# Optimization experiments

Hardware: AMD Instinct MI355X
Metric: run time of the kernel (lower is better)

The kernel has to match this reference:

```python
import jax, jax.numpy as jnp
import numpy as np

B, T, H = 128, 2048, 128

def setup_inputs() -> dict:
    key = jax.random.key(0)
    k1, k2, k3, k4, k5, k6 = jax.random.split(key, 6)
    s = 1.0 / np.sqrt(H)
    return {
        "H_pos": jax.random.normal(k1, (B, T, H), jnp.float32),
        "H_dyn": jax.random.normal(k2, (B, T, H), jnp.float32),
        "acc_w": jax.random.uniform(k3, (B, T), jnp.float32),
        "W_h": jax.random.uniform(k4, (H, H), jnp.float32, -s, s),
        "W_d": jax.random.uniform(k5, (H, H), jnp.float32, -s, s),
        "W_a": jax.random.uniform(k6, (H,), jnp.float32, -s, s),
        "b_a": jnp.zeros((), jnp.float32),
        "beta": jnp.zeros((), jnp.float32),
    }

def reference(H_pos, H_dyn, acc_w, W_h, W_d, W_a, b_a, beta):
    # energy: W_a(tanh(W_h H_pos + W_d H_dyn)) -> [B, T]
    z = jnp.tanh(jnp.einsum('bth,oh->bto', H_pos, W_h)
                 + jnp.einsum('bth,oh->bto', H_dyn, W_d))
    energy = jnp.einsum('bth,h->bt', z, W_a) + b_a
    # acceleration normalization
    acc_norm = acc_w / jnp.clip(jnp.max(acc_w, axis=1, keepdims=True), 1e-6)
    beta_pos = jax.nn.softplus(beta)
    alpha = jax.nn.softmax(energy * (1.0 + beta_pos * acc_norm), axis=1)  # [B, T]
    context = jnp.einsum('bt,bth->bh', alpha, H_pos)  # [B, H]
    return (context, alpha)
```

## Files before the change

kernel.cpp:

```cpp
#include <hip/hip_runtime.h>

#define B_ 128
#define T_ 2048
#define H_ 128
#define WPAD 136

typedef __attribute__((ext_vector_type(8))) short short8;
typedef __attribute__((ext_vector_type(4))) float f32x4;

__device__ __forceinline__ unsigned short f2b(float f) {
    unsigned int u = __float_as_uint(f);
    u += 0x7fffu + ((u >> 16) & 1u);
    return (unsigned short)(u >> 16);
}
__device__ __forceinline__ short8 pack8(const float4 x, const float4 y) {
    short8 r;
    r[0] = (short)f2b(x.x); r[1] = (short)f2b(x.y);
    r[2] = (short)f2b(x.z); r[3] = (short)f2b(x.w);
    r[4] = (short)f2b(y.x); r[5] = (short)f2b(y.y);
    r[6] = (short)f2b(y.z); r[7] = (short)f2b(y.w);
    return r;
}
__device__ __forceinline__ float tanh_fast(float x) {
    x = fminf(fmaxf(x, -20.f), 20.f);
    float e = __expf(2.f * x);
    return (e - 1.f) / (e + 1.f);
}

__global__ __launch_bounds__(256) void energy_kernel(
    const float* __restrict__ Hp,
    const float* __restrict__ Hd,
    const float* __restrict__ Wh,
    const float* __restrict__ Wd,
    const float* __restrict__ Wa,
    const float* __restrict__ ba_p,
    float* __restrict__ energy,
    int ntiles)
{
    __shared__ unsigned short Whs[H_ * WPAD];
    __shared__ unsigned short Wds[H_ * WPAD];
    __shared__ float Was[H_];

    const int tid = threadIdx.x;

    for (int i = tid; i < (H_ * H_) / 4; i += 256) {
        int row = i >> 5;
        int c4  = (i & 31) * 4;
        float4 wh = *(const float4*)&Wh[row * H_ + c4];
        float4 wd = *(const float4*)&Wd[row * H_ + c4];
        uint2 ph, pd;
        ph.x = (unsigned)f2b(wh.x) | ((unsigned)f2b(wh.y) << 16);
        ph.y = (unsigned)f2b(wh.z) | ((unsigned)f2b(wh.w) << 16);
        pd.x = (unsigned)f2b(wd.x) | ((unsigned)f2b(wd.y) << 16);
        pd.y = (unsigned)f2b(wd.z) | ((unsigned)f2b(wd.w) << 16);
        *(uint2*)&Whs[row * WPAD + c4] = ph;
        *(uint2*)&Wds[row * WPAD + c4] = pd;
    }
    if (tid < H_) Was[tid] = Wa[tid];
    __syncthreads();

    const float ba = ba_p[0];

    const int wave = tid >> 6;
    const int lane = tid & 63;
    const int l15  = lane & 15;
    const int lq   = lane >> 4;

    for (int tile = blockIdx.x; tile < ntiles; tile += gridDim.x) {
        const int row_base = tile * 64 + wave * 16;

        short8 afrag[8];
        const float* ap = Hp + (size_t)(row_base + l15) * H_ + lq * 8;
        const float* ad = Hd + (size_t)(row_base + l15) * H_ + lq * 8;
        #pragma unroll
        for (int kt = 0; kt < 4; kt++) {
            float4 x0 = *(const float4*)(ap + kt * 32);
            float4 x1 = *(const float4*)(ap + kt * 32 + 4);
            afrag[kt] = pack8(x0, x1);
            float4 y0 = *(const float4*)(ad + kt * 32);
            float4 y1 = *(const float4*)(ad + kt * 32 + 4);
            afrag[kt + 4] = pack8(y0, y1);
        }

        float ep[4] = {0.f, 0.f, 0.f, 0.f};
        #pragma unroll
        for (int nt = 0; nt < 8; nt++) {
            const int n = nt * 16 + l15;
            f32x4 acc = {0.f, 0.f, 0.f, 0.f};
            #pragma unroll
            for (int kt = 0; kt < 4; kt++) {
                short8 bf = *(const short8*)&Whs[n * WPAD + kt * 32 + lq * 8];
                acc = __builtin_amdgcn_mfma_f32_16x16x32_bf16(afrag[kt], bf, acc, 0, 0, 0);
            }
            #pragma unroll
            for (int kt = 0; kt < 4; kt++) {
                short8 bf = *(const short8*)&Wds[n * WPAD + kt * 32 + lq * 8];
                acc = __builtin_amdgcn_mfma_f32_16x16x32_bf16(afrag[kt + 4], bf, acc, 0, 0, 0);
            }
            const float wa = Was[n];
            #pragma unroll
            for (int r = 0; r < 4; r++) ep[r] += tanh_fast(acc[r]) * wa;
        }
        #pragma unroll
        for (int m = 1; m < 16; m <<= 1) {
            #pragma unroll
            for (int r = 0; r < 4; r++) ep[r] += __shfl_xor(ep[r], m, 64);
        }
        if (l15 == 0) {
            #pragma unroll
            for (int r = 0; r < 4; r++)
                energy[row_base + lq * 4 + r] = ep[r] + ba;
        }
    }
}

__global__ __launch_bounds__(256) void softmax_kernel(
    const float* __restrict__ accw,
    const float* __restrict__ beta_p,
    const float* __restrict__ energy,
    float* __restrict__ out_alpha)
{
    __shared__ float sred[8];
    const int b    = blockIdx.x;
    const int tid  = threadIdx.x;
    const int lane = tid & 63;
    const int wid  = tid >> 6;

    const float beta_pos = log1pf(__expf(beta_p[0]));

    float av[8], ev[8];
    float amax = -1e30f;
    #pragma unroll
    for (int i = 0; i < 8; i++) {
        int t = i * 256 + tid;
        av[i] = accw[b * T_ + t];
        ev[i] = energy[b * T_ + t];
        amax = fmaxf(amax, av[i]);
    }
    for (int m = 32; m >= 1; m >>= 1) amax = fmaxf(amax, __shfl_xor(amax, m, 64));
    if (lane == 0) sred[wid] = amax;
    __syncthreads();
    if (tid == 0)
        sred[4] = fmaxf(fmaxf(sred[0], sred[1]), fmaxf(sred[2], sred[3]));
    __syncthreads();
    const float invd = beta_pos / fmaxf(sred[4], 1e-6f);

    float sv[8], smax = -1e30f;
    #pragma unroll
    for (int i = 0; i < 8; i++) {
        sv[i] = ev[i] * (1.f + av[i] * invd);
        smax = fmaxf(smax, sv[i]);
    }
    for (int m = 32; m >= 1; m >>= 1) smax = fmaxf(smax, __shfl_xor(smax, m, 64));
    __syncthreads();
    if (lane == 0) sred[wid] = smax;
    __syncthreads();
    if (tid == 0)
        sred[5] = fmaxf(fmaxf(sred[0], sred[1]), fmaxf(sred[2], sred[3]));
    __syncthreads();
    const float smax_all = sred[5];

    float p[8], psum = 0.f;
    #pragma unroll
    for (int i = 0; i < 8; i++) { p[i] = __expf(sv[i] - smax_all); psum += p[i]; }
    for (int m = 32; m >= 1; m >>= 1) psum += __shfl_xor(psum, m, 64);
    __syncthreads();
    if (lane == 0) sred[wid] = psum;
    __syncthreads();
    if (tid == 0)
        sred[6] = sred[0] + sred[1] + sred[2] + sred[3];
    __syncthreads();
    const float invS = 1.f / sred[6];

    #pragma unroll
    for (int i = 0; i < 8; i++)
        out_alpha[b * T_ + i * 256 + tid] = p[i] * invS;
}

__global__ __launch_bounds__(256) void ctx_partial_kernel(
    const float* __restrict__ Hp,
    const float* __restrict__ alpha,
    float* __restrict__ cpart)
{
    __shared__ float red[32 * H_];
    __shared__ float red2[2 * H_];

    const int s   = blockIdx.x & 3;
    const int b   = blockIdx.x >> 2;
    const int tid = threadIdx.x;
    const int trow = tid >> 3;
    const int hseg = tid & 7;

    float c[16];
    #pragma unroll
    for (int j = 0; j < 16; j++) c[j] = 0.f;

    const float* base = Hp + ((size_t)b * T_ + s * 512) * H_ + hseg * 16;
    const float* al   = alpha + b * T_ + s * 512;

    for (int it = 0; it < 16; it++) {
        int t = it * 32 + trow;
        float a = al[t];
        const float* p0 = base + (size_t)t * H_;
        float4 v0 = *(const float4*)(p0);
        float4 v1 = *(const float4*)(p0 + 4);
        float4 v2 = *(const float4*)(p0 + 8);
        float4 v3 = *(const float4*)(p0 + 12);
        c[0]  += a * v0.x; c[1]  += a * v0.y; c[2]  += a * v0.z; c[3]  += a * v0.w;
        c[4]  += a * v1.x; c[5]  += a * v1.y; c[6]  += a * v1.z; c[7]  += a * v1.w;
        c[8]  += a * v2.x; c[9]  += a * v2.y; c[10] += a * v2.z; c[11] += a * v2.w;
        c[12] += a * v3.x; c[13] += a * v3.y; c[14] += a * v3.z; c[15] += a * v3.w;
    }
    #pragma unroll
    for (int j = 0; j < 16; j++) red[trow * H_ + hseg * 16 + j] = c[j];
    __syncthreads();
    {
        int h = tid & 127, half = tid >> 7;
        float ssum = 0.f;
        for (int r = half * 16; r < half * 16 + 16; r++) ssum += red[r * H_ + h];
        red2[half * H_ + h] = ssum;
    }
    __syncthreads();
    if (tid < H_)
        cpart[(b * 4 + s) * H_ + tid] = red2[tid] + red2[H_ + tid];
}

__global__ __launch_bounds__(256) void ctx_reduce_kernel(
    const float* __restrict__ cpart, float* __restrict__ out_ctx)
{
    int i = blockIdx.x * 256 + threadIdx.x;
    if (i < B_ * H_) {
        int b = i >> 7, h = i & 127;
        out_ctx[i] = cpart[(b * 4 + 0) * H_ + h] + cpart[(b * 4 + 1) * H_ + h]
                   + cpart[(b * 4 + 2) * H_ + h] + cpart[(b * 4 + 3) * H_ + h];
    }
}

extern "C" void kernel_launch(void* const* d_in, const int* in_sizes, int n_in,
                              void* d_out, int out_size, void* d_ws, size_t ws_size,
                              hipStream_t stream) {
    const float* Hp   = (const float*)d_in[0];
    const float* Hd   = (const float*)d_in[1];
    const float* accw = (const float*)d_in[2];
    const float* Wh   = (const float*)d_in[3];
    const float* Wd   = (const float*)d_in[4];
    const float* Wa   = (const float*)d_in[5];
    const float* ba   = (const float*)d_in[6];
    const float* beta = (const float*)d_in[7];

    float* energy_ws = (float*)d_ws;
    float* cpart_ws  = energy_ws + B_ * T_;

    float* out_ctx   = (float*)d_out;
    float* out_alpha = out_ctx + B_ * H_;

    const int ntiles = (B_ * T_) / 64;
    energy_kernel<<<1024, 256, 0, stream>>>(Hp, Hd, Wh, Wd, Wa, ba, energy_ws, ntiles);
    softmax_kernel<<<B_, 256, 0, stream>>>(accw, beta, energy_ws, out_alpha);
    ctx_partial_kernel<<<B_ * 4, 256, 0, stream>>>(Hp, out_alpha, cpart_ws);
    ctx_reduce_kernel<<<(B_ * H_ + 255) / 256, 256, 0, stream>>>(cpart_ws, out_ctx);
}
```

Baseline: 365.0 us.

## Enlarge energy blocks, interleave two MFMA chains, split context reduction finer

The energy kernel now uses 512-thread blocks with 128-row tiles, so each block loads and converts the shared bf16 weights over more rows. The inner loop now runs two independent MFMA accumulators per iteration to give the matrix unit more instruction-level parallelism. The context partial kernel splits each batch into 8 slices instead of 4 and stages alpha in shared memory, with simpler per-thread float4 accumulation. The aim is better weight amortization, MFMA latency hiding and more memory-level parallelism in the context pass, at the cost of higher register pressure and a larger partial buffer to reduce.

After: 514.6 us. 41.0% more time.

```diff
diff --git a/kernel.cpp b/kernel.cpp
--- a/kernel.cpp
+++ b/kernel.cpp
@@ -27,7 +27,7 @@
     return (e - 1.f) / (e + 1.f);
 }
 
-__global__ __launch_bounds__(256) void energy_kernel(
+__global__ __launch_bounds__(512, 4) void energy_kernel(
     const float* __restrict__ Hp,
     const float* __restrict__ Hd,
     const float* __restrict__ Wh,
@@ -43,7 +43,7 @@
 
     const int tid = threadIdx.x;
 
-    for (int i = tid; i < (H_ * H_) / 4; i += 256) {
+    for (int i = tid; i < (H_ * H_) / 4; i += 512) {
         int row = i >> 5;
         int c4  = (i & 31) * 4;
         float4 wh = *(const float4*)&Wh[row * H_ + c4];
@@ -67,7 +67,7 @@
     const int lq   = lane >> 4;
 
     for (int tile = blockIdx.x; tile < ntiles; tile += gridDim.x) {
-        const int row_base = tile * 64 + wave * 16;
+        const int row_base = tile * 128 + wave * 16;
 
         short8 afrag[8];
         const float* ap = Hp + (size_t)(row_base + l15) * H_ + lq * 8;
@@ -77,6 +77,9 @@
             float4 x0 = *(const float4*)(ap + kt * 32);
             float4 x1 = *(const float4*)(ap + kt * 32 + 4);
             afrag[kt] = pack8(x0, x1);
+        }
+        #pragma unroll
+        for (int kt = 0; kt < 4; kt++) {
             float4 y0 = *(const float4*)(ad + kt * 32);
             float4 y1 = *(const float4*)(ad + kt * 32 + 4);
             afrag[kt + 4] = pack8(y0, y1);
@@ -84,22 +87,25 @@
 
         float ep[4] = {0.f, 0.f, 0.f, 0.f};
         #pragma unroll
-        for (int nt = 0; nt < 8; nt++) {
-            const int n = nt * 16 + l15;
-            f32x4 acc = {0.f, 0.f, 0.f, 0.f};
-            #pragma unroll
-            for (int kt = 0; kt < 4; kt++) {
-                short8 bf = *(const short8*)&Whs[n * WPAD + kt * 32 + lq * 8];
-                acc = __builtin_amdgcn_mfma_f32_16x16x32_bf16(afrag[kt], bf, acc, 0, 0, 0);
+        for (int nt = 0; nt < 8; nt += 2) {
+            const int n0 = nt * 16 + l15;
+            const int n1 = n0 + 16;
+            f32x4 acc0 = {0.f, 0.f, 0.f, 0.f};
+            f32x4 acc1 = {0.f, 0.f, 0.f, 0.f};
+            #pragma unroll
+            for (int kt = 0; kt < 8; kt++) {
+                const unsigned short* ws = (kt < 4) ? Whs : Wds;
+                const int kk = (kt & 3) * 32 + lq * 8;
+                short8 b0 = *(const short8*)&ws[n0 * WPAD + kk];
+                short8 b1 = *(const short8*)&ws[n1 * WPAD + kk];
+                acc0 = __builtin_amdgcn_mfma_f32_16x16x32_bf16(afrag[kt], b0, acc0, 0, 0, 0);
+                acc1 = __builtin_amdgcn_mfma_f32_16x16x32_bf16(afrag[kt], b1, acc1, 0, 0, 0);
             }
-            #pragma unroll
-            for (int kt = 0; kt < 4; kt++) {
-                short8 bf = *(const short8*)&Wds[n * WPAD + kt * 32 + lq * 8];
-                acc = __builtin_amdgcn_mfma_f32_16x16x32_bf16(afrag[kt + 4], bf, acc, 0, 0, 0);
-            }
-            const float wa = Was[n];
-            #pragma unroll
-            for (int r = 0; r < 4; r++) ep[r] += tanh_fast(acc[r]) * wa;
+            const float wa0 = Was[n0];
+            const float wa1 = Was[n1];
+            #pragma unroll
+            for (int r = 0; r < 4; r++)
+                ep[r] += tanh_fast(acc0[r]) * wa0 + tanh_fast(acc1[r]) * wa1;
         }
         #pragma unroll
         for (int m = 1; m < 16; m <<= 1) {
@@ -182,47 +188,38 @@
     const float* __restrict__ alpha,
     float* __restrict__ cpart)
 {
-    __shared__ float red[32 * H_];
-    __shared__ float red2[2 * H_];
-
-    const int s   = blockIdx.x & 3;
-    const int b   = blockIdx.x >> 2;
+    __shared__ float al_s[256];
+    __shared__ float red[8 * H_];
+
+    const int sl  = blockIdx.x & 7;
+    const int b   = blockIdx.x >> 3;
     const int tid = threadIdx.x;
-    const int trow = tid >> 3;
-    const int hseg = tid & 7;
-
-    float c[16];
-    #pragma unroll
-    for (int j = 0; j < 16; j++) c[j] = 0.f;
-
-    const float* base = Hp + ((size_t)b * T_ + s * 512) * H_ + hseg * 16;
-    const float* al   = alpha + b * T_ + s * 512;
-
-    for (int it = 0; it < 16; it++) {
-        int t = it * 32 + trow;
-        float a = al[t];
-        const float* p0 = base + (size_t)t * H_;
-        float4 v0 = *(const float4*)(p0);
-        float4 v1 = *(const float4*)(p0 + 4);
-        float4 v2 = *(const float4*)(p0 + 8);
-        float4 v3 = *(const float4*)(p0 + 12);
-        c[0]  += a * v0.x; c[1]  += a * v0.y; c[2]  += a * v0.z; c[3]  += a * v0.w;
-        c[4]  += a * v1.x; c[5]  += a * v1.y; c[6]  += a * v1.z; c[7]  += a * v1.w;
-        c[8]  += a * v2.x; c[9]  += a * v2.y; c[10] += a * v2.z; c[11] += a * v2.w;
-        c[12] += a * v3.x; c[13] += a * v3.y; c[14] += a * v3.z; c[15] += a * v3.w;
-    }
-    #pragma unroll
-    for (int j = 0; j < 16; j++) red[trow * H_ + hseg * 16 + j] = c[j];
-    __syncthreads();
-    {
-        int h = tid & 127, half = tid >> 7;
-        float ssum = 0.f;
-        for (int r = half * 16; r < half * 16 + 16; r++) ssum += red[r * H_ + h];
-        red2[half * H_ + h] = ssum;
-    }
-    __syncthreads();
-    if (tid < H_)
-        cpart[(b * 4 + s) * H_ + tid] = red2[tid] + red2[H_ + tid];
+    const int row = tid >> 5;
+    const int c4  = tid & 31;
+
+    al_s[tid] = alpha[b * T_ + sl * 256 + tid];
+    __syncthreads();
+
+    float c0 = 0.f, c1 = 0.f, c2 = 0.f, c3 = 0.f;
+    const float* base = Hp + ((size_t)b * T_ + sl * 256) * H_ + c4 * 4;
+    #pragma unroll 4
+    for (int it = 0; it < 32; it++) {
+        int t = it * 8 + row;
+        float a = al_s[t];
+        float4 v = *(const float4*)(base + (size_t)t * H_);
+        c0 += a * v.x; c1 += a * v.y; c2 += a * v.z; c3 += a * v.w;
+    }
+    red[row * H_ + c4 * 4 + 0] = c0;
+    red[row * H_ + c4 * 4 + 1] = c1;
+    red[row * H_ + c4 * 4 + 2] = c2;
+    red[row * H_ + c4 * 4 + 3] = c3;
+    __syncthreads();
+    if (tid < H_) {
+        float s = 0.f;
+        #pragma unroll
+        for (int g = 0; g < 8; g++) s += red[g * H_ + tid];
+        cpart[(b * 8 + sl) * H_ + tid] = s;
+    }
 }
 
 __global__ __launch_bounds__(256) void ctx_reduce_kernel(
@@ -231,8 +228,10 @@
     int i = blockIdx.x * 256 + threadIdx.x;
     if (i < B_ * H_) {
         int b = i >> 7, h = i & 127;
-        out_ctx[i] = cpart[(b * 4 + 0) * H_ + h] + cpart[(b * 4 + 1) * H_ + h]
-                   + cpart[(b * 4 + 2) * H_ + h] + cpart[(b * 4 + 3) * H_ + h];
+        float s = 0.f;
+        #pragma unroll
+        for (int g = 0; g < 8; g++) s += cpart[(b * 8 + g) * H_ + h];
+        out_ctx[i] = s;
     }
 }
 
@@ -254,9 +253,9 @@
     float* out_ctx   = (float*)d_out;
     float* out_alpha = out_ctx + B_ * H_;
 
-    const int ntiles = (B_ * T_) / 64;
-    energy_kernel<<<1024, 256, 0, stream>>>(Hp, Hd, Wh, Wd, Wa, ba, energy_ws, ntiles);
+    const int ntiles = (B_ * T_) / 128;
+    energy_kernel<<<512, 512, 0, stream>>>(Hp, Hd, Wh, Wd, Wa, ba, energy_ws, ntiles);
     softmax_kernel<<<B_, 256, 0, stream>>>(accw, beta, energy_ws, out_alpha);
-    ctx_partial_kernel<<<B_ * 4, 256, 0, stream>>>(Hp, out_alpha, cpart_ws);
+    ctx_partial_kernel<<<B_ * 8, 256, 0, stream>>>(Hp, out_alpha, cpart_ws);
     ctx_reduce_kernel<<<(B_ * H_ + 255) / 256, 256, 0, stream>>>(cpart_ws, out_ctx);
 }
```
